# Kernel optimization log

Hardware: AMD Instinct MI355X
Metric: run time of the kernel (lower is better)

Reference implementation:

```python
import jax, jax.numpy as jnp
import numpy as np

B, N, C, H = 1, 128, 128, 8
D = C // H
SCALE = D ** -0.5


def layer_norm(x, w, b, eps=1e-5):
    m = jnp.mean(x, axis=-1, keepdims=True)
    v = jnp.var(x, axis=-1, keepdims=True)
    return (x - m) * jax.lax.rsqrt(v + eps) * w + b


def setup_inputs() -> dict:
    key = jax.random.key(0)
    ks = jax.random.split(key, 8)
    s = 0.02
    return {
        "e": jax.random.normal(ks[0], (B, N, N, C), jnp.float32),
        "mask": jnp.zeros((B, N, N, 1), jnp.float32),
        "ln_w": jnp.ones((C,), jnp.float32),
        "ln_b": jnp.zeros((C,), jnp.float32),
        "w_qkv_in": jax.random.normal(ks[1], (C, 3 * C), jnp.float32) * s,
        "b_qkv_in": jnp.zeros((3 * C,), jnp.float32),
        "w_eg_in": jax.random.normal(ks[2], (C, 2 * H), jnp.float32) * s,
        "b_eg_in": jnp.zeros((2 * H,), jnp.float32),
        "w_qkv_out": jax.random.normal(ks[3], (C, 3 * C), jnp.float32) * s,
        "b_qkv_out": jnp.zeros((3 * C,), jnp.float32),
        "w_eg_out": jax.random.normal(ks[4], (C, 2 * H), jnp.float32) * s,
        "b_eg_out": jnp.zeros((2 * H,), jnp.float32),
        "w_o": jax.random.normal(ks[5], (2 * C, C), jnp.float32) * s,
        "b_o": jnp.zeros((C,), jnp.float32),
    }


def reference(e, mask, ln_w, ln_b, w_qkv_in, b_qkv_in, w_eg_in, b_eg_in,
              w_qkv_out, b_qkv_out, w_eg_out, b_eg_out, w_o, b_o):
    b, n = e.shape[0], e.shape[1]
    e_ln = layer_norm(e, ln_w, ln_b)

    # ---- incoming-edge stream ----
    qkv = e_ln @ w_qkv_in + b_qkv_in                      # [b,n,n,3C]
    Q, K, V = jnp.split(qkv, 3, axis=-1)
    Q = Q.reshape(b, n, n, D, H) * SCALE                  # bijdh
    K = K.reshape(b, n, n, D, H)
    V = V.reshape(b, n, n, D, H)
    eg = e_ln @ w_eg_in + b_eg_in                         # [b,n,n,2H]
    E_in = eg[..., :H][:, :, None, :, :]                  # [b,i,1,k,h]
    G_in = eg[..., H:][:, :, None, :, :]
    H_in = jnp.einsum('bijdh,bjkdh->bijkh', Q, K) + E_in
    mask_in = mask[:, :, None, :, :]                      # [b,i,1,k,1]
    gates_in = jax.nn.sigmoid(G_in + mask_in)
    A_in = jax.nn.softmax(H_in + mask_in, axis=3) * gates_in
    Va_in = jnp.einsum('bijkh,bjkdh->bijdh', A_in, V)

    # ---- outgoing-edge stream ----
    qkv = e_ln @ w_qkv_out + b_qkv_out
    Q, K, V = jnp.split(qkv, 3, axis=-1)
    Q = Q.reshape(b, n, n, D, H) * SCALE
    K = K.reshape(b, n, n, D, H)
    V = V.reshape(b, n, n, D, H)
    eg = e_ln @ w_eg_out + b_eg_out
    E_out = eg[..., :H][:, :, :, None, :]                 # [b,k,i,1,h]
    G_out = eg[..., H:][:, :, :, None, :]
    H_out = jnp.einsum('bijdh,bkjdh->bkijh', Q, K) + E_out
    mask_out = mask[:, :, :, None, :]                     # [b,k,i,1,1]
    gates_out = jax.nn.sigmoid(G_out + mask_out)
    A_out = jax.nn.softmax(H_out + mask_out, axis=1) * gates_out
    Va_out = jnp.einsum('bkijh,bkjdh->bijdh', A_out, V)

    Va = jnp.concatenate([Va_in, Va_out], axis=-1).reshape(b, n, n, 2 * C)
    return Va @ w_o + b_o
```

## Files before the change

kernel.cpp:

```cpp
#include <hip/hip_runtime.h>
#include <hip/hip_bf16.h>


#define NPOS 16384
#define CDIM 128

typedef __attribute__((ext_vector_type(8))) short bf16x8;
typedef __attribute__((ext_vector_type(8))) unsigned short u16x8;
typedef __attribute__((ext_vector_type(4))) float f32x4;

#define MFMA16(a, b, c) __builtin_amdgcn_mfma_f32_16x16x32_bf16((a), (b), (c), 0, 0, 0)

#define GLL16(gp, lp) __builtin_amdgcn_global_load_lds( \
    (const __attribute__((address_space(1))) void*)(gp), \
    (__attribute__((address_space(3))) void*)(lp), 16, 0, 0)

static __device__ __forceinline__ unsigned short f2bf(float x) {
    union { float f; unsigned int u; } v; v.f = x;
    unsigned int u = v.u;
    unsigned int r = u + 0x7FFFu + ((u >> 16) & 1u);
    return (unsigned short)(r >> 16);
}
static __device__ __forceinline__ float bf2f(unsigned short h) {
    union { float f; unsigned int u; } v; v.u = ((unsigned int)h) << 16; return v.f;
}

__global__ __launch_bounds__(256) void prep_kernel(
    const float* __restrict__ e, const float* __restrict__ lnw,
    const float* __restrict__ lnb, unsigned short* __restrict__ e_hl,
    const float* __restrict__ wq1, const float* __restrict__ we1,
    unsigned short* __restrict__ B1t,
    const float* __restrict__ wq2, const float* __restrict__ we2,
    unsigned short* __restrict__ B2t,
    const float* __restrict__ wo, unsigned short* __restrict__ B3t)
{
    const int t = threadIdx.x;
    const int bx = blockIdx.x;
    if (bx < 4096) {
        const int lane = t & 63;
        const int row = bx * 4 + (t >> 6);
        float2 x = *(const float2*)(e + (size_t)row * CDIM + lane * 2);
        float s = x.x + x.y, s2 = x.x * x.x + x.y * x.y;
        #pragma unroll
        for (int off = 1; off < 64; off <<= 1) {
            s  += __shfl_xor(s,  off, 64);
            s2 += __shfl_xor(s2, off, 64);
        }
        float m = s * (1.f / 128.f);
        float v = s2 * (1.f / 128.f) - m * m;
        float sc = rsqrtf(v + 1e-5f);
        float2 wv = *(const float2*)(lnw + lane * 2);
        float2 bv = *(const float2*)(lnb + lane * 2);
        float y0 = (x.x - m) * sc * wv.x + bv.x;
        float y1 = (x.y - m) * sc * wv.y + bv.y;
        unsigned short h0 = f2bf(y0), h1 = f2bf(y1);
        ushort2 hi = {h0, h1};
        ushort2 lo = {f2bf(y0 - bf2f(h0)), f2bf(y1 - bf2f(h1))};
        *(ushort2*)(e_hl + (size_t)row * 256 + lane * 2)       = hi;
        *(ushort2*)(e_hl + (size_t)row * 256 + 128 + lane * 2) = lo;
    } else if (bx < 4544) {
        int pb = bx - 4096;
        const float* wq; const float* we; unsigned short* Bt;
        if (pb < 224) { wq = wq1; we = we1; Bt = B1t; }
        else          { pb -= 224; wq = wq2; we = we2; Bt = B2t; }
        const int idx = pb * 256 + t;
        const int n = idx >> 7, k = idx & 127;
        float v = 0.f;
        if (n < 384) v = wq[(size_t)k * 384 + n];
        else if (n < 400) v = we[(size_t)k * 16 + (n - 384)];
        unsigned short hi = f2bf(v);
        Bt[idx] = hi;
        Bt[448 * 128 + idx] = f2bf(v - bf2f(hi));
    } else {
        const int idx = (bx - 4544) * 256 + t;
        const int n = idx >> 8, kp = idx & 255;
        const int d = kp & 15, pl = kp >> 4;
        const int k = d * 16 + pl;
        float v = wo[(size_t)k * 128 + n];
        unsigned short hi = f2bf(v);
        B3t[idx] = hi;
        B3t[128 * 256 + idx] = f2bf(v - bf2f(hi));
    }
}

__global__ __launch_bounds__(256) void gemm_qkv_kernel(
    const unsigned short* __restrict__ e_hl,
    const unsigned short* __restrict__ B1t, const unsigned short* __restrict__ B2t,
    const float* __restrict__ bq_i, const float* __restrict__ be_i,
    const float* __restrict__ bq_o, const float* __restrict__ be_o,
    const float* __restrict__ mask,
    unsigned short* __restrict__ QT, unsigned short* __restrict__ KT,
    unsigned short* __restrict__ VT,
    unsigned short* __restrict__ Etab, unsigned short* __restrict__ Gtab)
{
    __shared__ __align__(16) unsigned char smem[24576];
    unsigned short* Alds = (unsigned short*)smem;
    unsigned short* Blds = (unsigned short*)(smem + 16384);

    const int t = threadIdx.x;
    const int wave = t >> 6, lane = t & 63;
    const int m = lane & 15, q = lane >> 4;
    const int c = blockIdx.x;
    const int bx = ((c & 31) << 2) | (c >> 5);
    const int W0blk = bx * 128;
    const int by = blockIdx.y;
    const int N0 = by * 64;
    const int br = blockIdx.z;
    const unsigned short* Bt = br ? B2t : B1t;
    const float* bias_qkv = br ? bq_o : bq_i;
    const float* bias_eg  = br ? be_o : be_i;

    f32x4 acc[2][4];
    #pragma unroll
    for (int a = 0; a < 2; ++a)
        #pragma unroll
        for (int cc = 0; cc < 4; ++cc) acc[a][cc] = (f32x4){0.f, 0.f, 0.f, 0.f};

    for (int kc = 0; kc < 4; ++kc) {
        #pragma unroll
        for (int ii = 0; ii < 6; ++ii) {
            const int id = wave + ii * 4;
            if (id < 16) {
                const int hl = id >> 3, s = id & 7;
                const int qq = s >> 1, rbase = (s & 1) * 64;
                const unsigned short* g = e_hl
                    + (size_t)(W0blk + rbase + lane) * 256 + hl * 128 + kc * 32 + qq * 8;
                unsigned short* l = Alds + hl * 4096 + qq * 1024 + rbase * 8;
                GLL16(g, l);
            } else {
                const int id2 = id - 16;
                const int hl = id2 >> 2, qq = id2 & 3;
                const unsigned short* g = Bt + (size_t)(N0 + lane) * 128
                    + hl * (448 * 128) + kc * 32 + qq * 8;
                unsigned short* l = Blds + hl * 2048 + qq * 512;
                GLL16(g, l);
            }
        }
        __syncthreads();

        bf16x8 aH[2], aL[2], bH[4], bL[4];
        #pragma unroll
        for (int ms = 0; ms < 2; ++ms) {
            const int row = wave * 32 + ms * 16 + m;
            aH[ms] = *(const bf16x8*)(Alds + 0    + q * 1024 + row * 8);
            aL[ms] = *(const bf16x8*)(Alds + 4096 + q * 1024 + row * 8);
        }
        #pragma unroll
        for (int ns = 0; ns < 4; ++ns) {
            bH[ns] = *(const bf16x8*)(Blds + 0    + q * 512 + (ns * 16 + m) * 8);
            bL[ns] = *(const bf16x8*)(Blds + 2048 + q * 512 + (ns * 16 + m) * 8);
        }
        #pragma unroll
        for (int ns = 0; ns < 4; ++ns) {
            acc[0][ns] = MFMA16(aH[0], bH[ns], acc[0][ns]);
            acc[1][ns] = MFMA16(aH[1], bH[ns], acc[1][ns]);
        }
        #pragma unroll
        for (int ns = 0; ns < 4; ++ns) {
            acc[0][ns] = MFMA16(aL[0], bH[ns], acc[0][ns]);
            acc[1][ns] = MFMA16(aL[1], bH[ns], acc[1][ns]);
        }
        #pragma unroll
        for (int ns = 0; ns < 4; ++ns) {
            acc[0][ns] = MFMA16(aH[0], bL[ns], acc[0][ns]);
            acc[1][ns] = MFMA16(aH[1], bL[ns], acc[1][ns]);
        }
        __syncthreads();
    }

    if (by < 6) {
        unsigned short (*Ts16)[66] = (unsigned short (*)[66])smem;
        #pragma unroll
        for (int ms = 0; ms < 2; ++ms)
            #pragma unroll
            for (int ns = 0; ns < 4; ++ns) {
                const int lc = ns * 16 + m;
                const int col = N0 + lc;
                const float bias = bias_qkv[col];
                const float scale = (col < 128) ? 0.25f : 1.f;
                #pragma unroll
                for (int r = 0; r < 4; ++r) {
                    const int lr = wave * 32 + ms * 16 + q * 4 + r;
                    Ts16[lr][lc] = f2bf((acc[ms][ns][r] + bias) * scale);
                }
            }
        __syncthreads();
        const int qsel = by >> 1, dhalf = by & 1;
        unsigned short* dstH = (qsel == 0) ? QT : (qsel == 1 ? KT : VT);
        const bool tr = (qsel == 0) || (br == 1);
        #pragma unroll
        for (int it = 0; it < 4; ++it) {
            int item = it * 256 + t;
            int hh = item >> 7, lr = item & 127;
            u16x8 hi;
            #pragma unroll
            for (int dd = 0; dd < 8; ++dd)
                hi[dd] = Ts16[lr][dd * 8 + hh];
            const size_t sub = ((size_t)(br * 8 + hh) * 2 + dhalf) * NPOS;
            const size_t p16 = tr ? ((size_t)lr * 128 + bx)
                                  : ((size_t)bx * 128 + lr);
            *(u16x8*)(dstH + (sub + p16) * 8) = hi;
        }
    } else {
        float* Tf = (float*)smem;
        #pragma unroll
        for (int ms = 0; ms < 2; ++ms) {
            const float bias = bias_eg[m];
            #pragma unroll
            for (int r = 0; r < 4; ++r) {
                const int lr = wave * 32 + ms * 16 + q * 4 + r;
                Tf[lr * 33 + m] = acc[ms][0][r] + bias;
            }
        }
        __syncthreads();
        const int r128 = t & 127, grp = t >> 7;
        const float mk = mask[bx * 128 + r128];
        const int dst = br ? (r128 * 128 + bx) : (bx * 128 + r128);
        if (grp == 0) {
            #pragma unroll
            for (int h = 0; h < 8; ++h)
                Etab[(size_t)(br * 8 + h) * NPOS + dst] =
                    f2bf(Tf[r128 * 33 + h] + mk);
        } else {
            #pragma unroll
            for (int h = 0; h < 8; ++h) {
                const float g = Tf[r128 * 33 + 8 + h] + mk;
                Gtab[(size_t)(br * 8 + h) * NPOS + dst] =
                    f2bf(1.f / (1.f + __expf(-g)));
            }
        }
    }
}

__global__ __launch_bounds__(256) void gemm_out_kernel(
    const float* __restrict__ va,
    const unsigned short* __restrict__ B3t,
    const float* __restrict__ bias,
    float* __restrict__ out)
{
    const int t = threadIdx.x;
    const int wave = t >> 6, lane = t & 63;
    const int m = lane & 15, q = lane >> 4;
    const int W0 = blockIdx.x * 64 + wave * 16;

    f32x4 acc[8];
    #pragma unroll
    for (int cc = 0; cc < 8; ++cc) acc[cc] = (f32x4){0.f, 0.f, 0.f, 0.f};

    const float* arow = va + (size_t)(W0 + m) * 256;
    const unsigned short* brow = B3t + (size_t)m * 256;

    #pragma unroll 2
    for (int kc = 0; kc < 8; ++kc) {
        const int ko = kc * 32 + q * 8;
        const float4* ap = (const float4*)(arow + ko);
        float4 f0 = ap[0], f1 = ap[1];
        float xs[8] = {f0.x, f0.y, f0.z, f0.w, f1.x, f1.y, f1.z, f1.w};
        bf16x8 ah, al;
        #pragma unroll
        for (int jj = 0; jj < 8; ++jj) {
            unsigned short h = f2bf(xs[jj]);
            ah[jj] = (short)h;
            al[jj] = (short)f2bf(xs[jj] - bf2f(h));
        }
        bf16x8 bh[8], bl[8];
        #pragma unroll
        for (int ns = 0; ns < 8; ++ns) {
            const unsigned short* bp = brow + (size_t)ns * (16 * 256) + ko;
            bh[ns] = *(const bf16x8*)bp;
            bl[ns] = *(const bf16x8*)(bp + 128 * 256);
        }
        #pragma unroll
        for (int ns = 0; ns < 8; ++ns) acc[ns] = MFMA16(ah, bh[ns], acc[ns]);
        #pragma unroll
        for (int ns = 0; ns < 8; ++ns) acc[ns] = MFMA16(al, bh[ns], acc[ns]);
        #pragma unroll
        for (int ns = 0; ns < 8; ++ns) acc[ns] = MFMA16(ah, bl[ns], acc[ns]);
    }

    #pragma unroll
    for (int ns = 0; ns < 8; ++ns) {
        const int col = ns * 16 + m;
        #pragma unroll
        for (int r = 0; r < 4; ++r) {
            const int prow = W0 + q * 4 + r;
            const int orow = ((prow & 127) << 7) | (prow >> 7);
            out[(size_t)orow * 128 + col] = acc[ns][r] + bias[col];
        }
    }
}

__global__ __launch_bounds__(256) void attn_kernel(
    const unsigned short* __restrict__ QT, const unsigned short* __restrict__ KT,
    const unsigned short* __restrict__ VT,
    const unsigned short* __restrict__ Etab, const unsigned short* __restrict__ Gtab,
    float* __restrict__ va)
{
    const int j = blockIdx.x, h = blockIdx.y, br = blockIdx.z;
    const int t = threadIdx.x;
    const int wave = t >> 6, lane = t & 63;
    const int m = lane & 15, q = lane >> 4;
    const int plane = br * 8 + h;
    const size_t SP = (size_t)NPOS * 8;
    const size_t jb = (size_t)j * 128 * 8;
    const unsigned short* __restrict__ Eb = Etab + (size_t)plane * NPOS;
    const unsigned short* __restrict__ Gb = Gtab + (size_t)plane * NPOS;

    __shared__ unsigned short Vth[16 * 136];
    __shared__ unsigned short Pl[128 * 136];

    const int strip = wave * 32;

    f32x4 S[2][8];
    #pragma unroll
    for (int mt = 0; mt < 2; ++mt)
        #pragma unroll
        for (int r = 0; r < 4; ++r) {
            const int i = strip + mt * 16 + q * 4 + r;
            u16x8 ev = *(const u16x8*)(Eb + (size_t)i * 128 + m * 8);
            #pragma unroll
            for (int nt = 0; nt < 8; ++nt) S[mt][nt][r] = bf2f(ev[nt]);
        }

    {
        int c = t >> 1, ch = t & 1;
        int krow = (c & 15) * 8 + (c >> 4);
        const unsigned short* src = VT + (size_t)(plane * 2 + ch) * SP + jb
                                  + (size_t)krow * 8;
        u16x8 v = *(const u16x8*)src;
        #pragma unroll
        for (int dd = 0; dd < 8; ++dd)
            Vth[(ch * 8 + dd) * 136 + c] = v[dd];
    }

    const bf16x8 zero8 = {};
    const int hf = q & 1;
    const size_t qko = (size_t)(plane * 2 + hf) * SP + jb;

    bf16x8 aQ[2];
    #pragma unroll
    for (int mt = 0; mt < 2; ++mt) {
        const size_t off = qko + (size_t)(strip + mt * 16 + m) * 8;
        aQ[mt] = (q < 2) ? *(const bf16x8*)(QT + off) : zero8;
    }

    #pragma unroll
    for (int nt = 0; nt < 8; ++nt) {
        const size_t koff = qko + (size_t)(m * 8 + nt) * 8;
        bf16x8 bK = (q < 2) ? *(const bf16x8*)(KT + koff) : zero8;
        #pragma unroll
        for (int mt = 0; mt < 2; ++mt)
            S[mt][nt] = MFMA16(aQ[mt], bK, S[mt][nt]);
    }

    #pragma unroll
    for (int mt = 0; mt < 2; ++mt)
        #pragma unroll
        for (int r = 0; r < 4; ++r) {
            float v = -1e30f;
            #pragma unroll
            for (int nt = 0; nt < 8; ++nt) v = fmaxf(v, S[mt][nt][r]);
            v = fmaxf(v, __shfl_xor(v, 1)); v = fmaxf(v, __shfl_xor(v, 2));
            v = fmaxf(v, __shfl_xor(v, 4)); v = fmaxf(v, __shfl_xor(v, 8));
            float s = 0.f;
            #pragma unroll
            for (int nt = 0; nt < 8; ++nt) {
                float p = __expf(S[mt][nt][r] - v);
                S[mt][nt][r] = p;
                s += p;
            }
            s += __shfl_xor(s, 1); s += __shfl_xor(s, 2);
            s += __shfl_xor(s, 4); s += __shfl_xor(s, 8);
            const float inv = 1.f / s;
            const int i = strip + mt * 16 + q * 4 + r;
            u16x8 gv = *(const u16x8*)(Gb + (size_t)i * 128 + m * 8);
            #pragma unroll
            for (int nt = 0; nt < 4; ++nt) {
                Pl[i * 136 + nt * 16 + m] =
                    f2bf(S[mt][nt][r] * inv * bf2f(gv[nt]));
                Pl[i * 136 + (nt + 4) * 16 + m] =
                    f2bf(S[mt][nt + 4][r] * inv * bf2f(gv[nt + 4]));
            }
        }

    __syncthreads();

    f32x4 av[2] = {(f32x4){0.f, 0.f, 0.f, 0.f}, (f32x4){0.f, 0.f, 0.f, 0.f}};
    #pragma unroll
    for (int kc = 0; kc < 4; ++kc) {
        const int off = kc * 32 + q * 8;
        bf16x8 bV = *(const bf16x8*)&Vth[m * 136 + off];
        #pragma unroll
        for (int mt = 0; mt < 2; ++mt) {
            bf16x8 aP = *(const bf16x8*)&Pl[(strip + mt * 16 + m) * 136 + off];
            av[mt] = MFMA16(aP, bV, av[mt]);
        }
    }

    #pragma unroll
    for (int mt = 0; mt < 2; ++mt)
        #pragma unroll
        for (int r = 0; r < 4; ++r) {
            const int i = strip + mt * 16 + q * 4 + r;
            va[((size_t)(j * 128 + i)) * 256 + plane * 16 + m] = av[mt][r];
        }
}

extern "C" void kernel_launch(void* const* d_in, const int* in_sizes, int n_in,
                              void* d_out, int out_size, void* d_ws, size_t ws_size,
                              hipStream_t stream) {
    const float* e        = (const float*)d_in[0];
    const float* mask     = (const float*)d_in[1];
    const float* ln_w     = (const float*)d_in[2];
    const float* ln_b     = (const float*)d_in[3];
    const float* w_qkv_in = (const float*)d_in[4];
    const float* b_qkv_in = (const float*)d_in[5];
    const float* w_eg_in  = (const float*)d_in[6];
    const float* b_eg_in  = (const float*)d_in[7];
    const float* w_qkv_o  = (const float*)d_in[8];
    const float* b_qkv_o  = (const float*)d_in[9];
    const float* w_eg_o   = (const float*)d_in[10];
    const float* b_eg_o   = (const float*)d_in[11];
    const float* w_o      = (const float*)d_in[12];
    const float* b_o      = (const float*)d_in[13];
    float* out = (float*)d_out;

    char* base = (char*)d_ws;
    const size_t PLANE = (size_t)16 * NPOS * 16;
    unsigned short* e_hl = (unsigned short*)base;
    unsigned short* QT = (unsigned short*)(base + (size_t)NPOS * 256 * 2);
    unsigned short* KT = QT + PLANE;
    unsigned short* VT = KT + PLANE;
    float* va = (float*)(VT + PLANE);
    unsigned short* Etab = (unsigned short*)(va + (size_t)NPOS * 256);
    unsigned short* Gtab = Etab + (size_t)16 * NPOS;
    unsigned short* B3t  = Gtab + (size_t)16 * NPOS;

    unsigned short* B1t = (unsigned short*)va;
    unsigned short* B2t = B1t + (size_t)2 * 448 * 128;

    prep_kernel<<<4672, 256, 0, stream>>>(
        e, ln_w, ln_b, e_hl,
        w_qkv_in, w_eg_in, B1t, w_qkv_o, w_eg_o, B2t, w_o, B3t);

    gemm_qkv_kernel<<<dim3(128, 7, 2), 256, 0, stream>>>(
        e_hl, B1t, B2t, b_qkv_in, b_eg_in, b_qkv_o, b_eg_o, mask,
        QT, KT, VT, Etab, Gtab);

    attn_kernel<<<dim3(128, 8, 2), 256, 0, stream>>>(
        QT, KT, VT, Etab, Gtab, va);

    gemm_out_kernel<<<256, 256, 0, stream>>>(va, B3t, b_o, out);
}
```

Measured before the change: 167.7 us.

## Reuse E/G tiles across two j per attention block and pre-split va to bf16 hi/lo

Result: slower. 185.7 us (+10.7%).

```diff
diff --git a/kernel.cpp b/kernel.cpp
--- a/kernel.cpp
+++ b/kernel.cpp
@@ -232,8 +232,143 @@
     }
 }
 
+__global__ __launch_bounds__(256) void attn_kernel(
+    const unsigned short* __restrict__ QT, const unsigned short* __restrict__ KT,
+    const unsigned short* __restrict__ VT,
+    const unsigned short* __restrict__ Etab, const unsigned short* __restrict__ Gtab,
+    unsigned short* __restrict__ vaH, unsigned short* __restrict__ vaL)
+{
+    const int bid = blockIdx.x;
+    const int plane = bid >> 6;
+    const int j0 = (bid & 63) * 2;
+    const int t = threadIdx.x;
+    const int wave = t >> 6, lane = t & 63;
+    const int m = lane & 15, q = lane >> 4;
+    const size_t SP = (size_t)NPOS * 8;
+    const unsigned short* __restrict__ Eb = Etab + (size_t)plane * NPOS;
+    const unsigned short* __restrict__ Gb = Gtab + (size_t)plane * NPOS;
+
+    __shared__ unsigned short Vth[16 * 136];
+    __shared__ unsigned short Pl[128 * 136];
+
+    const int strip = wave * 32;
+
+    u16x8 Ec[2][4], Gc[2][4];
+    #pragma unroll
+    for (int mt = 0; mt < 2; ++mt)
+        #pragma unroll
+        for (int r = 0; r < 4; ++r) {
+            const int i = strip + mt * 16 + q * 4 + r;
+            Ec[mt][r] = *(const u16x8*)(Eb + (size_t)i * 128 + m * 8);
+            Gc[mt][r] = *(const u16x8*)(Gb + (size_t)i * 128 + m * 8);
+        }
+
+    for (int it = 0; it < 2; ++it) {
+        const int j = j0 + it;
+        const size_t jb = (size_t)j * 128 * 8;
+
+        f32x4 S[2][8];
+        #pragma unroll
+        for (int mt = 0; mt < 2; ++mt)
+            #pragma unroll
+            for (int r = 0; r < 4; ++r) {
+                #pragma unroll
+                for (int nt = 0; nt < 8; ++nt)
+                    S[mt][nt][r] = bf2f(Ec[mt][r][nt]);
+            }
+
+        {
+            int c = t >> 1, ch = t & 1;
+            int krow = (c & 15) * 8 + (c >> 4);
+            const unsigned short* src = VT + (size_t)(plane * 2 + ch) * SP + jb
+                                      + (size_t)krow * 8;
+            u16x8 v = *(const u16x8*)src;
+            #pragma unroll
+            for (int dd = 0; dd < 8; ++dd)
+                Vth[(ch * 8 + dd) * 136 + c] = v[dd];
+        }
+
+        const bf16x8 zero8 = {};
+        const int hf = q & 1;
+        const size_t qko = (size_t)(plane * 2 + hf) * SP + jb;
+
+        bf16x8 aQ[2];
+        #pragma unroll
+        for (int mt = 0; mt < 2; ++mt) {
+            const size_t off = qko + (size_t)(strip + mt * 16 + m) * 8;
+            aQ[mt] = (q < 2) ? *(const bf16x8*)(QT + off) : zero8;
+        }
+
+        #pragma unroll
+        for (int nt = 0; nt < 8; ++nt) {
+            const size_t koff = qko + (size_t)(m * 8 + nt) * 8;
+            bf16x8 bK = (q < 2) ? *(const bf16x8*)(KT + koff) : zero8;
+            #pragma unroll
+            for (int mt = 0; mt < 2; ++mt)
+                S[mt][nt] = MFMA16(aQ[mt], bK, S[mt][nt]);
+        }
+
+        #pragma unroll
+        for (int mt = 0; mt < 2; ++mt)
+            #pragma unroll
+            for (int r = 0; r < 4; ++r) {
+                float v = -1e30f;
+                #pragma unroll
+                for (int nt = 0; nt < 8; ++nt) v = fmaxf(v, S[mt][nt][r]);
+                v = fmaxf(v, __shfl_xor(v, 1)); v = fmaxf(v, __shfl_xor(v, 2));
+                v = fmaxf(v, __shfl_xor(v, 4)); v = fmaxf(v, __shfl_xor(v, 8));
+                float s = 0.f;
+                #pragma unroll
+                for (int nt = 0; nt < 8; ++nt) {
+                    float p = __expf(S[mt][nt][r] - v);
+                    S[mt][nt][r] = p;
+                    s += p;
+                }
+                s += __shfl_xor(s, 1); s += __shfl_xor(s, 2);
+                s += __shfl_xor(s, 4); s += __shfl_xor(s, 8);
+                const float inv = 1.f / s;
+                const int i = strip + mt * 16 + q * 4 + r;
+                #pragma unroll
+                for (int nt = 0; nt < 4; ++nt) {
+                    Pl[i * 136 + nt * 16 + m] =
+                        f2bf(S[mt][nt][r] * inv * bf2f(Gc[mt][r][nt]));
+                    Pl[i * 136 + (nt + 4) * 16 + m] =
+                        f2bf(S[mt][nt + 4][r] * inv * bf2f(Gc[mt][r][nt + 4]));
+                }
+            }
+
+        __syncthreads();
+
+        f32x4 av[2] = {(f32x4){0.f, 0.f, 0.f, 0.f}, (f32x4){0.f, 0.f, 0.f, 0.f}};
+        #pragma unroll
+        for (int kc = 0; kc < 4; ++kc) {
+            const int off = kc * 32 + q * 8;
+            bf16x8 bV = *(const bf16x8*)&Vth[m * 136 + off];
+            #pragma unroll
+            for (int mt = 0; mt < 2; ++mt) {
+                bf16x8 aP = *(const bf16x8*)&Pl[(strip + mt * 16 + m) * 136 + off];
+                av[mt] = MFMA16(aP, bV, av[mt]);
+            }
+        }
+
+        #pragma unroll
+        for (int mt = 0; mt < 2; ++mt)
+            #pragma unroll
+            for (int r = 0; r < 4; ++r) {
+                const int i = strip + mt * 16 + q * 4 + r;
+                const size_t addr = ((size_t)(j * 128 + i)) * 256 + plane * 16 + m;
+                const float x = av[mt][r];
+                const unsigned short hi = f2bf(x);
+                vaH[addr] = hi;
+                vaL[addr] = f2bf(x - bf2f(hi));
+            }
+        __syncthreads();
+    }
+}
+
 __global__ __launch_bounds__(256) void gemm_out_kernel(
-    const float* __restrict__ va,
+    const unsigned short* __restrict__ vaH,
+    const unsigned short* __restrict__ vaL,
     const unsigned short* __restrict__ B3t,
     const float* __restrict__ bias,
     float* __restrict__ out)
@@ -241,46 +376,42 @@
     const int t = threadIdx.x;
     const int wave = t >> 6, lane = t & 63;
     const int m = lane & 15, q = lane >> 4;
-    const int W0 = blockIdx.x * 64 + wave * 16;
-
-    f32x4 acc[8];
+    const int W0 = (blockIdx.x >> 1) * 64 + wave * 16;
+    const int N0 = (blockIdx.x & 1) * 64;
+
+    f32x4 acc[4];
     #pragma unroll
-    for (int cc = 0; cc < 8; ++cc) acc[cc] = (f32x4){0.f, 0.f, 0.f, 0.f};
-
-    const float* arow = va + (size_t)(W0 + m) * 256;
-    const unsigned short* brow = B3t + (size_t)m * 256;
+    for (int cc = 0; cc < 4; ++cc) acc[cc] = (f32x4){0.f, 0.f, 0.f, 0.f};
+
+    const unsigned short* arowH = vaH + (size_t)(W0 + m) * 256;
+    const unsigned short* arowL = vaL + (size_t)(W0 + m) * 256;
+    const unsigned short* bcol[4];
+    #pragma unroll
+    for (int ns = 0; ns < 4; ++ns)
+        bcol[ns] = B3t + (size_t)(N0 + ns * 16 + m) * 256;
 
     #pragma unroll 2
     for (int kc = 0; kc < 8; ++kc) {
         const int ko = kc * 32 + q * 8;
-        const float4* ap = (const float4*)(arow + ko);
-        float4 f0 = ap[0], f1 = ap[1];
-        float xs[8] = {f0.x, f0.y, f0.z, f0.w, f1.x, f1.y, f1.z, f1.w};
-        bf16x8 ah, al;
-        #pragma unroll
-        for (int jj = 0; jj < 8; ++jj) {
-            unsigned short h = f2bf(xs[jj]);
-            ah[jj] = (short)h;
-            al[jj] = (short)f2bf(xs[jj] - bf2f(h));
-        }
-        bf16x8 bh[8], bl[8];
-        #pragma unroll
-        for (int ns = 0; ns < 8; ++ns) {
-            const unsigned short* bp = brow + (size_t)ns * (16 * 256) + ko;
-            bh[ns] = *(const bf16x8*)bp;
-            bl[ns] = *(const bf16x8*)(bp + 128 * 256);
-        }
-        #pragma unroll
-        for (int ns = 0; ns < 8; ++ns) acc[ns] = MFMA16(ah, bh[ns], acc[ns]);
-        #pragma unroll
-        for (int ns = 0; ns < 8; ++ns) acc[ns] = MFMA16(al, bh[ns], acc[ns]);
-        #pragma unroll
-        for (int ns = 0; ns < 8; ++ns) acc[ns] = MFMA16(ah, bl[ns], acc[ns]);
+        bf16x8 ah = *(const bf16x8*)(arowH + ko);
+        bf16x8 al = *(const bf16x8*)(arowL + ko);
+        bf16x8 bh[4], bl[4];
+        #pragma unroll
+        for (int ns = 0; ns < 4; ++ns) {
+            bh[ns] = *(const bf16x8*)(bcol[ns] + ko);
+            bl[ns] = *(const bf16x8*)(bcol[ns] + 128 * 256 + ko);
+        }
+        #pragma unroll
+        for (int ns = 0; ns < 4; ++ns) acc[ns] = MFMA16(ah, bh[ns], acc[ns]);
+        #pragma unroll
+        for (int ns = 0; ns < 4; ++ns) acc[ns] = MFMA16(al, bh[ns], acc[ns]);
+        #pragma unroll
+        for (int ns = 0; ns < 4; ++ns) acc[ns] = MFMA16(ah, bl[ns], acc[ns]);
     }
 
     #pragma unroll
-    for (int ns = 0; ns < 8; ++ns) {
-        const int col = ns * 16 + m;
+    for (int ns = 0; ns < 4; ++ns) {
+        const int col = N0 + ns * 16 + m;
         #pragma unroll
         for (int r = 0; r < 4; ++r) {
             const int prow = W0 + q * 4 + r;
@@ -288,122 +419,6 @@
             out[(size_t)orow * 128 + col] = acc[ns][r] + bias[col];
         }
     }
-}
-
-__global__ __launch_bounds__(256) void attn_kernel(
-    const unsigned short* __restrict__ QT, const unsigned short* __restrict__ KT,
-    const unsigned short* __restrict__ VT,
-    const unsigned short* __restrict__ Etab, const unsigned short* __restrict__ Gtab,
-    float* __restrict__ va)
-{
-    const int j = blockIdx.x, h = blockIdx.y, br = blockIdx.z;
-    const int t = threadIdx.x;
-    const int wave = t >> 6, lane = t & 63;
-    const int m = lane & 15, q = lane >> 4;
-    const int plane = br * 8 + h;
-    const size_t SP = (size_t)NPOS * 8;
-    const size_t jb = (size_t)j * 128 * 8;
-    const unsigned short* __restrict__ Eb = Etab + (size_t)plane * NPOS;
-    const unsigned short* __restrict__ Gb = Gtab + (size_t)plane * NPOS;
-
-    __shared__ unsigned short Vth[16 * 136];
-    __shared__ unsigned short Pl[128 * 136];
-
-    const int strip = wave * 32;
-
-    f32x4 S[2][8];
-    #pragma unroll
-    for (int mt = 0; mt < 2; ++mt)
-        #pragma unroll
-        for (int r = 0; r < 4; ++r) {
-            const int i = strip + mt * 16 + q * 4 + r;
-            u16x8 ev = *(const u16x8*)(Eb + (size_t)i * 128 + m * 8);
-            #pragma unroll
-            for (int nt = 0; nt < 8; ++nt) S[mt][nt][r] = bf2f(ev[nt]);
-        }
-
-    {
-        int c = t >> 1, ch = t & 1;
-        int krow = (c & 15) * 8 + (c >> 4);
-        const unsigned short* src = VT + (size_t)(plane * 2 + ch) * SP + jb
-                                  + (size_t)krow * 8;
-        u16x8 v = *(const u16x8*)src;
-        #pragma unroll
-        for (int dd = 0; dd < 8; ++dd)
-            Vth[(ch * 8 + dd) * 136 + c] = v[dd];
-    }
-
-    const bf16x8 zero8 = {};
-    const int hf = q & 1;
-    const size_t qko = (size_t)(plane * 2 + hf) * SP + jb;
-
-    bf16x8 aQ[2];
-    #pragma unroll
-    for (int mt = 0; mt < 2; ++mt) {
-        const size_t off = qko + (size_t)(strip + mt * 16 + m) * 8;
-        aQ[mt] = (q < 2) ? *(const bf16x8*)(QT + off) : zero8;
-    }
-
-    #pragma unroll
-    for (int nt = 0; nt < 8; ++nt) {
-        const size_t koff = qko + (size_t)(m * 8 + nt) * 8;
-        bf16x8 bK = (q < 2) ? *(const bf16x8*)(KT + koff) : zero8;
-        #pragma unroll
-        for (int mt = 0; mt < 2; ++mt)
-            S[mt][nt] = MFMA16(aQ[mt], bK, S[mt][nt]);
-    }
-
-    #pragma unroll
-    for (int mt = 0; mt < 2; ++mt)
-        #pragma unroll
-        for (int r = 0; r < 4; ++r) {
-            float v = -1e30f;
-            #pragma unroll
-            for (int nt = 0; nt < 8; ++nt) v = fmaxf(v, S[mt][nt][r]);
-            v = fmaxf(v, __shfl_xor(v, 1)); v = fmaxf(v, __shfl_xor(v, 2));
-            v = fmaxf(v, __shfl_xor(v, 4)); v = fmaxf(v, __shfl_xor(v, 8));
-            float s = 0.f;
-            #pragma unroll
-            for (int nt = 0; nt < 8; ++nt) {
-                float p = __expf(S[mt][nt][r] - v);
-                S[mt][nt][r] = p;
-                s += p;
-            }
-            s += __shfl_xor(s, 1); s += __shfl_xor(s, 2);
-            s += __shfl_xor(s, 4); s += __shfl_xor(s, 8);
-            const float inv = 1.f / s;
-            const int i = strip + mt * 16 + q * 4 + r;
-            u16x8 gv = *(const u16x8*)(Gb + (size_t)i * 128 + m * 8);
-            #pragma unroll
-            for (int nt = 0; nt < 4; ++nt) {
-                Pl[i * 136 + nt * 16 + m] =
-                    f2bf(S[mt][nt][r] * inv * bf2f(gv[nt]));
-                Pl[i * 136 + (nt + 4) * 16 + m] =
-                    f2bf(S[mt][nt + 4][r] * inv * bf2f(gv[nt + 4]));
-            }
-        }
-
-    __syncthreads();
-
-    f32x4 av[2] = {(f32x4){0.f, 0.f, 0.f, 0.f}, (f32x4){0.f, 0.f, 0.f, 0.f}};
-    #pragma unroll
-    for (int kc = 0; kc < 4; ++kc) {
-        const int off = kc * 32 + q * 8;
-        bf16x8 bV = *(const bf16x8*)&Vth[m * 136 + off];
-        #pragma unroll
-        for (int mt = 0; mt < 2; ++mt) {
-            bf16x8 aP = *(const bf16x8*)&Pl[(strip + mt * 16 + m) * 136 + off];
-            av[mt] = MFMA16(aP, bV, av[mt]);
-        }
-    }
-
-    #pragma unroll
-    for (int mt = 0; mt < 2; ++mt)
-        #pragma unroll
-        for (int r = 0; r < 4; ++r) {
-            const int i = strip + mt * 16 + q * 4 + r;
-            va[((size_t)(j * 128 + i)) * 256 + plane * 16 + m] = av[mt][r];
-        }
 }
 
 extern "C" void kernel_launch(void* const* d_in, const int* in_sizes, int n_in,
@@ -431,12 +446,13 @@
     unsigned short* QT = (unsigned short*)(base + (size_t)NPOS * 256 * 2);
     unsigned short* KT = QT + PLANE;
     unsigned short* VT = KT + PLANE;
-    float* va = (float*)(VT + PLANE);
-    unsigned short* Etab = (unsigned short*)(va + (size_t)NPOS * 256);
+    unsigned short* vaH = VT + PLANE;
+    unsigned short* vaL = vaH + (size_t)NPOS * 256;
+    unsigned short* Etab = vaL + (size_t)NPOS * 256;
     unsigned short* Gtab = Etab + (size_t)16 * NPOS;
     unsigned short* B3t  = Gtab + (size_t)16 * NPOS;
 
-    unsigned short* B1t = (unsigned short*)va;
+    unsigned short* B1t = vaH;
     unsigned short* B2t = B1t + (size_t)2 * 448 * 128;
 
     prep_kernel<<<4672, 256, 0, stream>>>(
@@ -447,8 +463,8 @@
         e_hl, B1t, B2t, b_qkv_in, b_eg_in, b_qkv_o, b_eg_o, mask,
         QT, KT, VT, Etab, Gtab);
 
-    attn_kernel<<<dim3(128, 8, 2), 256, 0, stream>>>(
-        QT, KT, VT, Etab, Gtab, va);
-
-    gemm_out_kernel<<<256, 256, 0, stream>>>(va, B3t, b_o, out);
-}
+    attn_kernel<<<1024, 256, 0, stream>>>(
+        QT, KT, VT, Etab, Gtab, vaH, vaL);
+
+    gemm_out_kernel<<<512, 256, 0, stream>>>(vaH, vaL, B3t, b_o, out);
+}
```
